# Optimization experiments

Measured on AMD Instinct MI355X. Metric: run time of the kernel, lower is better.

Reference implementation:

```python
import jax, jax.numpy as jnp
import numpy as np

DIM = 3072
NUM_HEADS = 24
HEAD_DIM = 128
SEQ = 2048
BATCH = 1
EPS = 1e-6


def _make_rope(seq_len: int, head_dim: int):
    # Standard RoPE angles; cos/sin laid out per interleaved-pair convention
    # (each frequency repeated for the (real, imag) pair), shape [S, head_dim].
    half = head_dim // 2
    inv_freq = 1.0 / (10000.0 ** (np.arange(0, half, dtype=np.float32) / half))
    t = np.arange(seq_len, dtype=np.float32)
    freqs = np.outer(t, inv_freq)  # [S, half]
    freqs = np.repeat(freqs, 2, axis=-1)  # [S, head_dim], pairs share the angle
    return jnp.asarray(np.cos(freqs)), jnp.asarray(np.sin(freqs))


def setup_inputs() -> dict:
    key = jax.random.key(0)
    ks = jax.random.split(key, 8)
    inner = NUM_HEADS * HEAD_DIM
    s = 0.02
    hidden_states = jax.random.normal(ks[0], (BATCH, SEQ, DIM), dtype=jnp.float32)
    wq = jax.random.normal(ks[1], (inner, DIM), dtype=jnp.float32) * s
    wk = jax.random.normal(ks[2], (inner, DIM), dtype=jnp.float32) * s
    wv = jax.random.normal(ks[3], (inner, DIM), dtype=jnp.float32) * s
    bq = jax.random.normal(ks[4], (inner,), dtype=jnp.float32) * s
    bk = jax.random.normal(ks[5], (inner,), dtype=jnp.float32) * s
    bv = jax.random.normal(ks[6], (inner,), dtype=jnp.float32) * s
    norm_q_w = jnp.ones((HEAD_DIM,), dtype=jnp.float32)
    norm_k_w = jnp.ones((HEAD_DIM,), dtype=jnp.float32)
    cos, sin = _make_rope(SEQ, HEAD_DIM)
    return {
        "hidden_states": hidden_states,
        "wq": wq, "bq": bq, "wk": wk, "bk": bk, "wv": wv, "bv": bv,
        "norm_q_w": norm_q_w, "norm_k_w": norm_k_w,
        "cos": cos, "sin": sin,
    }


def _rms_norm(x, w, eps=EPS):
    # RMSNorm over the last (head_dim) axis.
    var = jnp.mean(jnp.square(x), axis=-1, keepdims=True)
    return x * jax.lax.rsqrt(var + eps) * w


def _apply_rope(x, cos, sin):
    # x: [B, S, H, D]; cos/sin: [S, D]. Interleaved-pair rotation
    # (diffusers apply_rotary_emb, use_real_unbind_dim=-1).
    xr = x[..., 0::2]
    xi = x[..., 1::2]
    rot = jnp.stack([-xi, xr], axis=-1).reshape(x.shape)
    c = cos[None, :, None, :]
    s = sin[None, :, None, :]
    return x * c + rot * s


def reference(hidden_states, wq, bq, wk, bk, wv, bv, norm_q_w, norm_k_w, cos, sin):
    B, S, _ = hidden_states.shape
    H, D = NUM_HEADS, HEAD_DIM
    # QKV projections (ColumnParallelLinear with tp_size=1)
    q = (hidden_states @ wq.T + bq).reshape(B, S, H, D)
    k = (hidden_states @ wk.T + bk).reshape(B, S, H, D)
    v = (hidden_states @ wv.T + bv).reshape(B, S, H, D)
    # qk-norm then RoPE
    q = _apply_rope(_rms_norm(q, norm_q_w), cos, sin)
    k = _apply_rope(_rms_norm(k, norm_k_w), cos, sin)
    # Non-causal full attention
    scale = 1.0 / jnp.sqrt(jnp.asarray(D, dtype=q.dtype))
    scores = jnp.einsum("bqhd,bkhd->bhqk", q, k) * scale
    probs = jax.nn.softmax(scores, axis=-1)
    out = jnp.einsum("bhqk,bkhd->bqhd", probs, v)
    return out.reshape(B, S, H * D).astype(q.dtype)
```

## Files before the change

### kernel.cpp

```cpp
#include <hip/hip_runtime.h>

#define S_LEN 2048
#define DIMSZ 3072
#define NHEAD 24
#define HDIM 128
#define NQKV 9216
#define QSCALE 0.08838834764831845f
#define FMAX 12.0f

typedef unsigned short u16;
typedef unsigned int u32;
typedef __attribute__((ext_vector_type(8))) short short8;
typedef __attribute__((ext_vector_type(4))) float f32x4;

__device__ __forceinline__ u16 f2bf(float f) {
    u32 u = __float_as_uint(f);
    u32 r = (u + 0x7fffu + ((u >> 16) & 1u)) >> 16;
    return (u16)r;
}
__device__ __forceinline__ float bf2f(u16 u) {
    return __uint_as_float((u32)u << 16);
}

__device__ __forceinline__ void lds16(u16* lds, const u16* g) {
    __builtin_amdgcn_global_load_lds((const __attribute__((address_space(1))) u32*)g,
                                     (__attribute__((address_space(3))) u32*)lds, 16, 0, 0);
}

__global__ void k_f2bf4(const float4* __restrict__ src, u16* __restrict__ dst, int n4) {
    int i = blockIdx.x * blockDim.x + threadIdx.x;
    if (i >= n4) return;
    float4 v = src[i];
    u32 lo = (u32)f2bf(v.x) | ((u32)f2bf(v.y) << 16);
    u32 hi = (u32)f2bf(v.z) | ((u32)f2bf(v.w) << 16);
    uint2 p; p.x = lo; p.y = hi;
    *(uint2*)(dst + (size_t)i * 4) = p;
}

__global__ __launch_bounds__(512, 1) void k_gemm(const u16* __restrict__ A, const u16* __restrict__ W,
                                                 u16* __restrict__ C) {
    __shared__ __align__(16) u16 As[2][256 * 64];
    __shared__ __align__(16) u16 Bs[2][320 * 64];
    const int tid = threadIdx.x, wave = tid >> 6, lane = tid & 63;
    const int bm = blockIdx.x & 7, bn = blockIdx.x >> 3;
    const int wm = wave >> 1, wn = wave & 1;
    const int frow = lane & 15, fk = lane >> 4;
    const u16* baseA = A + (size_t)(bm * 256) * DIMSZ;
    const u16* baseW = W + (size_t)(bn * 288) * DIMSZ;

    auto stageA = [&](int b, int kt) {
#pragma unroll
        for (int j = 0; j < 4; ++j) {
            int flat = j * 512 + tid, row = flat >> 3, ch = flat & 7;
            lds16(&As[b][flat * 8], baseA + (size_t)row * DIMSZ + kt * 64 + ((ch ^ (row & 7)) * 8));
        }
    };
    auto stageB = [&](int b, int kt) {
#pragma unroll
        for (int j = 0; j < 5; ++j) {
            int flat = j * 512 + tid, row = flat >> 3, ch = flat & 7;
            int srow = bn * 288 + row;
            srow = (srow > NQKV - 1) ? (NQKV - 1) : srow;
            lds16(&Bs[b][flat * 8], W + (size_t)srow * DIMSZ + kt * 64 + ((ch ^ (row & 7)) * 8));
        }
    };

    stageA(0, 0); stageB(0, 0); stageA(1, 1); stageB(1, 1);
    asm volatile("s_waitcnt vmcnt(9)");
    __builtin_amdgcn_s_barrier();

    f32x4 acc[4][9] = {};
    for (int T = 0; T < 48; ++T) {
        const int b = T & 1;
        const u16* LA = As[b];
        const u16* LB = Bs[b];
        short8 af[4][2];
#pragma unroll
        for (int mf = 0; mf < 4; ++mf) {
            int lrow = wm * 64 + mf * 16 + frow;
#pragma unroll
            for (int ks = 0; ks < 2; ++ks)
                af[mf][ks] = *(const short8*)&LA[lrow * 64 + (((ks * 4 + fk) ^ (frow & 7)) * 8)];
        }
#pragma unroll
        for (int ph = 0; ph < 3; ++ph) {
            short8 bf[3][2];
#pragma unroll
            for (int j = 0; j < 3; ++j) {
                int nf = ph * 3 + j;
                int lrow = wn * 144 + nf * 16 + frow;
#pragma unroll
                for (int ks = 0; ks < 2; ++ks)
                    bf[j][ks] = *(const short8*)&LB[lrow * 64 + (((ks * 4 + fk) ^ (frow & 7)) * 8)];
            }
            __builtin_amdgcn_s_barrier();
            __builtin_amdgcn_s_setprio(1);
#pragma unroll
            for (int mf = 0; mf < 4; ++mf)
#pragma unroll
                for (int j = 0; j < 3; ++j)
#pragma unroll
                    for (int ks = 0; ks < 2; ++ks)
                        acc[mf][ph * 3 + j] =
                            __builtin_amdgcn_mfma_f32_16x16x32_bf16(af[mf][ks], bf[j][ks], acc[mf][ph * 3 + j], 0, 0, 0);
            __builtin_amdgcn_s_setprio(0);
            __builtin_amdgcn_s_barrier();
        }
        if (T < 46) {
            stageB(b, T + 2);
            stageA(b, T + 2);
            asm volatile("s_waitcnt vmcnt(9)");
            __builtin_amdgcn_s_barrier();
        } else if (T == 46) {
            asm volatile("s_waitcnt vmcnt(0)");
            __builtin_amdgcn_s_barrier();
        }
    }

#pragma unroll
    for (int mf = 0; mf < 4; ++mf) {
#pragma unroll
        for (int nf = 0; nf < 9; ++nf) {
            int n = bn * 288 + wn * 144 + nf * 16 + frow;
#pragma unroll
            for (int i = 0; i < 4; ++i) {
                int m = bm * 256 + wm * 64 + mf * 16 + fk * 4 + i;
                C[(size_t)m * NQKV + n] = f2bf(acc[mf][nf][i]);
            }
        }
    }
}

__global__ void k_post(const u16* __restrict__ qkv, const float* __restrict__ nw_q,
                       const float* __restrict__ nw_k, const float* __restrict__ bq,
                       const float* __restrict__ bk, const float* __restrict__ bv,
                       const float* __restrict__ cosT, const float* __restrict__ sinT,
                       u16* __restrict__ Qb, u16* __restrict__ Kb, u16* __restrict__ Vt) {
    const int wave = threadIdx.x >> 6, lane = threadIdx.x & 63;
    const int s = blockIdx.x * 4 + wave;
    const int h = blockIdx.y;
    const int d0 = 2 * lane, d1 = 2 * lane + 1;
    const float c = cosT[s * HDIM + d0], sn = sinT[s * HDIM + d0];
    const u16* r0 = qkv + (size_t)s * NQKV + h * HDIM;
    {
        float x0 = bf2f(r0[d0]) + bq[h * HDIM + d0];
        float x1 = bf2f(r0[d1]) + bq[h * HDIM + d1];
        float ss = x0 * x0 + x1 * x1;
        for (int m = 1; m < 64; m <<= 1) ss += __shfl_xor(ss, m);
        float r = rsqrtf(ss * (1.0f / 128.0f) + 1e-6f);
        x0 *= r * nw_q[d0]; x1 *= r * nw_q[d1];
        float o0 = (x0 * c - x1 * sn) * QSCALE;
        float o1 = (x1 * c + x0 * sn) * QSCALE;
        u32 p = (u32)f2bf(o0) | ((u32)f2bf(o1) << 16);
        *(u32*)&Qb[((size_t)h * S_LEN + s) * HDIM + d0] = p;
    }
    {
        float x0 = bf2f(r0[3072 + d0]) + bk[h * HDIM + d0];
        float x1 = bf2f(r0[3072 + d1]) + bk[h * HDIM + d1];
        float ss = x0 * x0 + x1 * x1;
        for (int m = 1; m < 64; m <<= 1) ss += __shfl_xor(ss, m);
        float r = rsqrtf(ss * (1.0f / 128.0f) + 1e-6f);
        x0 *= r * nw_k[d0]; x1 *= r * nw_k[d1];
        float o0 = x0 * c - x1 * sn;
        float o1 = x1 * c + x0 * sn;
        u32 p = (u32)f2bf(o0) | ((u32)f2bf(o1) << 16);
        *(u32*)&Kb[((size_t)h * S_LEN + s) * HDIM + d0] = p;
    }
    {
        float v0 = bf2f(r0[6144 + d0]) + bv[h * HDIM + d0];
        float v1 = bf2f(r0[6144 + d1]) + bv[h * HDIM + d1];
        Vt[((size_t)h * HDIM + d0) * S_LEN + s] = f2bf(v0);
        Vt[((size_t)h * HDIM + d1) * S_LEN + s] = f2bf(v1);
    }
}

__global__ __launch_bounds__(256, 2) void k_attn(const u16* __restrict__ Qb, const u16* __restrict__ Kb,
                                                 const u16* __restrict__ Vt, float* __restrict__ out) {
    __shared__ __align__(16) u16 Ks[2][64 * 128];
    __shared__ __align__(16) u16 Vs[2][128 * 64];
    __shared__ __align__(16) u16 Ps[4][32 * 64];
    const int wave = threadIdx.x >> 6, lane = threadIdx.x & 63;
    const int wg = (blockIdx.x & 7) * 48 + (blockIdx.x >> 3);
    const int h = wg >> 4, qb = wg & 15;
    const int frow = lane & 15, fk = lane >> 4;

    short8 qf[2][4];
#pragma unroll
    for (int qg = 0; qg < 2; ++qg) {
        const u16* qbase = Qb + ((size_t)h * S_LEN + qb * 128 + wave * 32 + qg * 16 + frow) * HDIM + fk * 8;
#pragma unroll
        for (int ks = 0; ks < 4; ++ks) qf[qg][ks] = *(const short8*)(qbase + ks * 32);
    }

    f32x4 o[2][8] = {};
    float l_p[2][4] = {};

#define STAGE(buf, kt)                                                                       \
    {                                                                                        \
        _Pragma("unroll") for (int c = 0; c < 4; ++c) {                                      \
            int fi = (wave * 4 + c) * 64 + lane;                                             \
            {                                                                                \
                int r = fi >> 4, ch = fi & 15;                                               \
                lds16(Ks[buf] + (wave * 4 + c) * 512,                                        \
                      Kb + ((size_t)h * S_LEN + (kt) * 64 + r) * HDIM + ((ch ^ (r & 15)) * 8)); \
            }                                                                                \
            {                                                                                \
                int r = fi >> 3, ch = fi & 7;                                                \
                lds16(Vs[buf] + (wave * 4 + c) * 512,                                        \
                      Vt + ((size_t)h * HDIM + r) * S_LEN + (kt) * 64 + ((ch ^ (r & 7)) * 8)); \
            }                                                                                \
        }                                                                                    \
    }

    STAGE(0, 0);
    __syncthreads();
    int cur = 0;

    for (int kt = 0; kt < S_LEN / 64; ++kt) {
        if (kt + 1 < S_LEN / 64) STAGE(cur ^ 1, kt + 1);
        f32x4 sacc[2][4] = {};
#pragma unroll
        for (int nf = 0; nf < 4; ++nf) {
#pragma unroll
            for (int ks = 0; ks < 4; ++ks) {
                short8 kf = *(const short8*)&Ks[cur][(nf * 16 + frow) * 128 + (((ks * 4 + fk) ^ frow) & 15) * 8];
#pragma unroll
                for (int qg = 0; qg < 2; ++qg)
                    sacc[qg][nf] = __builtin_amdgcn_mfma_f32_16x16x32_bf16(qf[qg][ks], kf, sacc[qg][nf], 0, 0, 0);
            }
        }
#pragma unroll
        for (int qg = 0; qg < 2; ++qg)
#pragma unroll
            for (int nf = 0; nf < 4; ++nf)
#pragma unroll
                for (int i = 0; i < 4; ++i) {
                    float p = __expf(sacc[qg][nf][i] - FMAX);
                    l_p[qg][i] += p;
                    int row = qg * 16 + fk * 4 + i, col = nf * 16 + frow;
                    Ps[wave][row * 64 + (((col >> 3) ^ (row & 7)) << 3) + (col & 7)] = f2bf(p);
                }
#pragma unroll
        for (int ks = 0; ks < 2; ++ks) {
            short8 pf[2];
#pragma unroll
            for (int qg = 0; qg < 2; ++qg)
                pf[qg] = *(const short8*)&Ps[wave][(qg * 16 + frow) * 64 + (((ks * 4 + fk) ^ (frow & 7)) & 7) * 8];
#pragma unroll
            for (int nf8 = 0; nf8 < 8; ++nf8) {
                short8 vf = *(const short8*)&Vs[cur][(nf8 * 16 + frow) * 64 + (((ks * 4 + fk) ^ (frow & 7)) & 7) * 8];
#pragma unroll
                for (int qg = 0; qg < 2; ++qg)
                    o[qg][nf8] = __builtin_amdgcn_mfma_f32_16x16x32_bf16(pf[qg], vf, o[qg][nf8], 0, 0, 0);
            }
        }
        __syncthreads();
        cur ^= 1;
    }
#undef STAGE

#pragma unroll
    for (int msk = 1; msk < 16; msk <<= 1)
#pragma unroll
        for (int qg = 0; qg < 2; ++qg)
#pragma unroll
            for (int i = 0; i < 4; ++i) l_p[qg][i] += __shfl_xor(l_p[qg][i], msk);

#pragma unroll
    for (int qg = 0; qg < 2; ++qg)
#pragma unroll
        for (int nf8 = 0; nf8 < 8; ++nf8)
#pragma unroll
            for (int i = 0; i < 4; ++i) {
                int srow = qb * 128 + wave * 32 + qg * 16 + fk * 4 + i;
                out[(size_t)srow * DIMSZ + h * HDIM + nf8 * 16 + frow] = o[qg][nf8][i] / l_p[qg][i];
            }
}

extern "C" void kernel_launch(void* const* d_in, const int* in_sizes, int n_in,
                              void* d_out, int out_size, void* d_ws, size_t ws_size,
                              hipStream_t stream) {
    const float* hs = (const float*)d_in[0];
    const float* wq = (const float*)d_in[1];
    const float* bq = (const float*)d_in[2];
    const float* wk = (const float*)d_in[3];
    const float* bk = (const float*)d_in[4];
    const float* wv = (const float*)d_in[5];
    const float* bv = (const float*)d_in[6];
    const float* nq = (const float*)d_in[7];
    const float* nk = (const float*)d_in[8];
    const float* cosT = (const float*)d_in[9];
    const float* sinT = (const float*)d_in[10];
    float* out = (float*)d_out;

    char* ws = (char*)d_ws;
    const size_t HS_B = 12582912, W_B = 56623104, QKV_B = 37748736;
    u16* hs_b = (u16*)(ws);
    u16* w_b = (u16*)(ws + HS_B);
    u16* qkv = (u16*)(ws + HS_B + W_B);
    char* tail = ws + HS_B + W_B + QKV_B;
    u16* Qb = (u16*)(tail);
    u16* Kb = (u16*)(tail + 12582912);
    u16* Vt = (u16*)(tail + 25165824);

    k_f2bf4<<<6144, 256, 0, stream>>>((const float4*)hs, hs_b, 1572864);
    k_f2bf4<<<9216, 256, 0, stream>>>((const float4*)wq, w_b, 2359296);
    k_f2bf4<<<9216, 256, 0, stream>>>((const float4*)wk, w_b + 9437184, 2359296);
    k_f2bf4<<<9216, 256, 0, stream>>>((const float4*)wv, w_b + 18874368, 2359296);

    k_gemm<<<dim3(256), 512, 0, stream>>>(hs_b, w_b, qkv);

    k_post<<<dim3(512, 24), 256, 0, stream>>>(qkv, nq, nk, bq, bk, bv, cosT, sinT, Qb, Kb, Vt);

    k_attn<<<dim3(384), 256, 0, stream>>>(Qb, Kb, Vt, out);
}
```

Before: 318.7 us.

## Retile QKV GEMM to 256x144 blocks with BK=32 and two blocks per CU

The QKV projection GEMM changes from 512-thread blocks computing 256x288 tiles with K-step 64 to 256-thread blocks computing 256x144 tiles with K-step 32. The grid doubles to 512 blocks, LDS use per block drops, and launch bounds now allow two blocks per CU. The LDS swizzle is rewritten for the 32-wide rows. The aim is more concurrency to hide latency and better load balance across CUs, at the cost of more barriers per K and lower arithmetic intensity per block, since A tiles are reloaded for twice as many N-blocks.

```diff
diff --git a/kernel.cpp b/kernel.cpp
--- a/kernel.cpp
+++ b/kernel.cpp
@@ -37,81 +37,66 @@
     *(uint2*)(dst + (size_t)i * 4) = p;
 }
 
-__global__ __launch_bounds__(512, 1) void k_gemm(const u16* __restrict__ A, const u16* __restrict__ W,
+__global__ __launch_bounds__(256, 2) void k_gemm(const u16* __restrict__ A, const u16* __restrict__ W,
                                                  u16* __restrict__ C) {
-    __shared__ __align__(16) u16 As[2][256 * 64];
-    __shared__ __align__(16) u16 Bs[2][320 * 64];
+    __shared__ __align__(16) u16 As[2][256 * 32];
+    __shared__ __align__(16) u16 Bs[2][192 * 32];
     const int tid = threadIdx.x, wave = tid >> 6, lane = tid & 63;
     const int bm = blockIdx.x & 7, bn = blockIdx.x >> 3;
-    const int wm = wave >> 1, wn = wave & 1;
     const int frow = lane & 15, fk = lane >> 4;
     const u16* baseA = A + (size_t)(bm * 256) * DIMSZ;
-    const u16* baseW = W + (size_t)(bn * 288) * DIMSZ;
 
     auto stageA = [&](int b, int kt) {
 #pragma unroll
         for (int j = 0; j < 4; ++j) {
-            int flat = j * 512 + tid, row = flat >> 3, ch = flat & 7;
-            lds16(&As[b][flat * 8], baseA + (size_t)row * DIMSZ + kt * 64 + ((ch ^ (row & 7)) * 8));
+            int flat = j * 256 + tid, row = flat >> 2, ch = flat & 3;
+            lds16(&As[b][flat * 8], baseA + (size_t)row * DIMSZ + kt * 32 + ((ch ^ ((row >> 1) & 3)) * 8));
         }
     };
     auto stageB = [&](int b, int kt) {
 #pragma unroll
-        for (int j = 0; j < 5; ++j) {
-            int flat = j * 512 + tid, row = flat >> 3, ch = flat & 7;
-            int srow = bn * 288 + row;
+        for (int j = 0; j < 3; ++j) {
+            int flat = j * 256 + tid, row = flat >> 2, ch = flat & 3;
+            int srow = bn * 144 + row;
             srow = (srow > NQKV - 1) ? (NQKV - 1) : srow;
-            lds16(&Bs[b][flat * 8], W + (size_t)srow * DIMSZ + kt * 64 + ((ch ^ (row & 7)) * 8));
+            lds16(&Bs[b][flat * 8], W + (size_t)srow * DIMSZ + kt * 32 + ((ch ^ ((row >> 1) & 3)) * 8));
         }
     };
 
     stageA(0, 0); stageB(0, 0); stageA(1, 1); stageB(1, 1);
-    asm volatile("s_waitcnt vmcnt(9)");
+    asm volatile("s_waitcnt vmcnt(7)");
     __builtin_amdgcn_s_barrier();
 
     f32x4 acc[4][9] = {};
-    for (int T = 0; T < 48; ++T) {
+    for (int T = 0; T < 96; ++T) {
         const int b = T & 1;
         const u16* LA = As[b];
         const u16* LB = Bs[b];
-        short8 af[4][2];
+        short8 af[4], bf[9];
 #pragma unroll
         for (int mf = 0; mf < 4; ++mf) {
-            int lrow = wm * 64 + mf * 16 + frow;
-#pragma unroll
-            for (int ks = 0; ks < 2; ++ks)
-                af[mf][ks] = *(const short8*)&LA[lrow * 64 + (((ks * 4 + fk) ^ (frow & 7)) * 8)];
-        }
-#pragma unroll
-        for (int ph = 0; ph < 3; ++ph) {
-            short8 bf[3][2];
-#pragma unroll
-            for (int j = 0; j < 3; ++j) {
-                int nf = ph * 3 + j;
-                int lrow = wn * 144 + nf * 16 + frow;
-#pragma unroll
-                for (int ks = 0; ks < 2; ++ks)
-                    bf[j][ks] = *(const short8*)&LB[lrow * 64 + (((ks * 4 + fk) ^ (frow & 7)) * 8)];
-            }
+            int row = wave * 64 + mf * 16 + frow;
+            af[mf] = *(const short8*)&LA[row * 32 + ((fk ^ ((row >> 1) & 3)) * 8)];
+        }
+#pragma unroll
+        for (int nf = 0; nf < 9; ++nf) {
+            int row = nf * 16 + frow;
+            bf[nf] = *(const short8*)&LB[row * 32 + ((fk ^ ((row >> 1) & 3)) * 8)];
+        }
+        __builtin_amdgcn_s_barrier();
+        __builtin_amdgcn_s_setprio(1);
+#pragma unroll
+        for (int mf = 0; mf < 4; ++mf)
+#pragma unroll
+            for (int nf = 0; nf < 9; ++nf)
+                acc[mf][nf] = __builtin_amdgcn_mfma_f32_16x16x32_bf16(af[mf], bf[nf], acc[mf][nf], 0, 0, 0);
+        __builtin_amdgcn_s_setprio(0);
+        __builtin_amdgcn_s_barrier();
+        if (T < 94) {
+            stageA(b, T + 2); stageB(b, T + 2);
+            asm volatile("s_waitcnt vmcnt(7)");
             __builtin_amdgcn_s_barrier();
-            __builtin_amdgcn_s_setprio(1);
-#pragma unroll
-            for (int mf = 0; mf < 4; ++mf)
-#pragma unroll
-                for (int j = 0; j < 3; ++j)
-#pragma unroll
-                    for (int ks = 0; ks < 2; ++ks)
-                        acc[mf][ph * 3 + j] =
-                            __builtin_amdgcn_mfma_f32_16x16x32_bf16(af[mf][ks], bf[j][ks], acc[mf][ph * 3 + j], 0, 0, 0);
-            __builtin_amdgcn_s_setprio(0);
-            __builtin_amdgcn_s_barrier();
-        }
-        if (T < 46) {
-            stageB(b, T + 2);
-            stageA(b, T + 2);
-            asm volatile("s_waitcnt vmcnt(9)");
-            __builtin_amdgcn_s_barrier();
-        } else if (T == 46) {
+        } else if (T == 94) {
             asm volatile("s_waitcnt vmcnt(0)");
             __builtin_amdgcn_s_barrier();
         }
@@ -121,10 +106,10 @@
     for (int mf = 0; mf < 4; ++mf) {
 #pragma unroll
         for (int nf = 0; nf < 9; ++nf) {
-            int n = bn * 288 + wn * 144 + nf * 16 + frow;
+            int n = bn * 144 + nf * 16 + frow;
 #pragma unroll
             for (int i = 0; i < 4; ++i) {
-                int m = bm * 256 + wm * 64 + mf * 16 + fk * 4 + i;
+                int m = bm * 256 + wave * 64 + mf * 16 + fk * 4 + i;
                 C[(size_t)m * NQKV + n] = f2bf(acc[mf][nf][i]);
             }
         }
@@ -308,7 +293,7 @@
     k_f2bf4<<<9216, 256, 0, stream>>>((const float4*)wk, w_b + 9437184, 2359296);
     k_f2bf4<<<9216, 256, 0, stream>>>((const float4*)wv, w_b + 18874368, 2359296);
 
-    k_gemm<<<dim3(256), 512, 0, stream>>>(hs_b, w_b, qkv);
+    k_gemm<<<dim3(512), 256, 0, stream>>>(hs_b, w_b, qkv);
 
     k_post<<<dim3(512, 24), 256, 0, stream>>>(qkv, nq, nk, bq, bk, bv, cosT, sinT, Qb, Kb, Vt);
 
```

New measurement: 310.2 us. 2.7% less time.
